# Performance work log

Hardware: AMD Instinct MI355X
Metric: run time of the kernel (lower is better)

The kernel has to match this reference:

```python
import jax, jax.numpy as jnp
import numpy as np

TOKENS = 32768
D_MODEL = 4096
N_EXPERTS = 64
BALANCE_LOSS_WEIGHT = 0.1


def setup_inputs() -> dict:
    key = jax.random.key(0)
    kx, kw1, kw2, kn = jax.random.split(key, 4)
    x = jax.random.normal(kx, (TOKENS, D_MODEL), dtype=jnp.float32)
    # torch nn.Linear weight layout: [out_features, in_features]
    w1 = jax.random.normal(kw1, (N_EXPERTS, D_MODEL), dtype=jnp.float32) / np.sqrt(D_MODEL)
    w2 = jax.random.normal(kw2, (N_EXPERTS, N_EXPERTS), dtype=jnp.float32) / np.sqrt(N_EXPERTS)
    # fixed Gumbel noise sample: g = -log(-log(u)), matching gumbel_rsample
    u = jax.random.uniform(kn, (TOKENS, N_EXPERTS), dtype=jnp.float32, minval=1e-8, maxval=1.0)
    noise = -jnp.log(-jnp.log(u))
    return {"x": x, "w1": w1, "w2": w2, "noise": noise}


def reference(x, w1, w2, noise):
    # MLP gate: Linear(d->E, no bias) -> tanh -> Linear(E->E, no bias)
    h = jnp.tanh(x @ w1.T)                       # [T, E]
    logits = h @ w2.T                             # [T, E]
    scores = jax.nn.softmax(logits, axis=1)       # [T, E]
    logits_w_noise = logits + noise               # gumbel-perturbed logits
    top1_indices = jnp.argmax(logits_w_noise, axis=1)   # [T] int
    top1_scores = jnp.max(logits_w_noise, axis=1)       # [T]
    # balance loss
    importance_mean = scores.mean(axis=0)                        # [E]
    load = jnp.bincount(top1_indices, length=N_EXPERTS)          # [E] int
    load_mean = load.astype(scores.dtype) / x.shape[0]           # [E]
    balance_loss = (N_EXPERTS * jnp.sum(importance_mean * load_mean)
                    * BALANCE_LOSS_WEIGHT)
    return (top1_indices, top1_scores, balance_loss, load_mean, importance_mean)
```

## Files before the change

kernel.cpp:

```cpp
#include <hip/hip_runtime.h>
#include <math.h>

#define TOKENS 32768
#define DM 4096
#define NE 64
#define BALW 0.1f

#define TG 64
#define GBLOCKS (TOKENS / TG)

typedef __attribute__((ext_vector_type(8))) short short8;
typedef __attribute__((ext_vector_type(4))) float f32x4;

typedef unsigned short us;

__device__ inline us bf16r(float f) {
  const unsigned u = __float_as_uint(f);
  return (us)((u + 0x7FFFu + ((u >> 16) & 1u)) >> 16);
}
__device__ inline float bf16f(us s) {
  return __uint_as_float(((unsigned)s) << 16);
}
__device__ inline void split8(const float4 v0, const float4 v1, short8& H,
                              short8& M, short8& L) {
  float v[8] = {v0.x, v0.y, v0.z, v0.w, v1.x, v1.y, v1.z, v1.w};
#pragma unroll
  for (int j = 0; j < 8; ++j) {
    const us hs = bf16r(v[j]);
    const float r1 = v[j] - bf16f(hs);
    const us ms = bf16r(r1);
    const float r2 = r1 - bf16f(ms);
    const us ls = bf16r(r2);
    H[j] = (short)hs; M[j] = (short)ms; L[j] = (short)ls;
  }
}

#define MFMA(a, b, c) __builtin_amdgcn_mfma_f32_16x16x32_bf16(a, b, c, 0, 0, 0)

__global__ void prep_w1_kernel(const float* __restrict__ w1,
                               us* __restrict__ bws) {
  const int kc = blockIdx.x;
  const int tid = threadIdx.x;
  const int ns = tid >> 6;
  const int l = tid & 63;
  const int r = l & 15, g = l >> 4;
  const int n = 16 * ns + r;
  const int kb = 32 * kc + 8 * g;
  const float* src = &w1[(size_t)n * DM + kb];
  const float4 v0 = *reinterpret_cast<const float4*>(src);
  const float4 v1 = *reinterpret_cast<const float4*>(src + 4);
  short8 H, M, L;
  split8(v0, v1, H, M, L);
  us* dst = bws + ((size_t)(kc * 4 + ns) * 3) * 512 + l * 8;
  *reinterpret_cast<short8*>(dst) = H;
  *reinterpret_cast<short8*>(dst + 512) = M;
  *reinterpret_cast<short8*>(dst + 1024) = L;
}

#define TMM 128

template <int SK>
__global__ __launch_bounds__(256, 3) void gemm_mfma_kernel(
    const float* __restrict__ x, const us* __restrict__ bws,
    float* __restrict__ hp) {
  constexpr int KS = DM / SK;
  constexpr int NIT = KS / 32;
  const int tid = threadIdx.x;
  const int kz = blockIdx.x % SK;
  const int mb = blockIdx.x / SK;
  const int w = tid >> 6;
  const int l = tid & 63;
  const int r = l & 15, g = l >> 4;
  const int row0 = mb * TMM + w * 32;
  const int kb0 = kz * KS;

  f32x4 acc[2][4];
#pragma unroll
  for (int i = 0; i < 2; ++i)
#pragma unroll
    for (int j = 0; j < 4; ++j) acc[i][j] = (f32x4)(0.f);

  const float* xA0 = &x[(size_t)(row0 + r) * DM + kb0 + 8 * g];
  const float* xA1 = xA0 + (size_t)16 * DM;
  const us* bb = bws + (size_t)(kb0 / 32) * 12 * 512 + l * 8;

  for (int it = 0; it < NIT; ++it) {
    const int koff = it * 32;
    const float4 a00 = *reinterpret_cast<const float4*>(xA0 + koff);
    const float4 a01 = *reinterpret_cast<const float4*>(xA0 + koff + 4);
    const float4 a10 = *reinterpret_cast<const float4*>(xA1 + koff);
    const float4 a11 = *reinterpret_cast<const float4*>(xA1 + koff + 4);
    const us* bt = bb + (size_t)it * 12 * 512;
    short8 bf[4][3];
#pragma unroll
    for (int ns = 0; ns < 4; ++ns)
#pragma unroll
      for (int p = 0; p < 3; ++p)
        bf[ns][p] =
            *reinterpret_cast<const short8*>(bt + (ns * 3 + p) * 512);

    short8 ah, am, al;
    split8(a00, a01, ah, am, al);
#pragma unroll
    for (int ns = 0; ns < 4; ++ns) {
      f32x4 c = acc[0][ns];
      c = MFMA(ah, bf[ns][0], c);
      c = MFMA(ah, bf[ns][1], c);
      c = MFMA(am, bf[ns][0], c);
      c = MFMA(ah, bf[ns][2], c);
      c = MFMA(am, bf[ns][1], c);
      c = MFMA(al, bf[ns][0], c);
      c = MFMA(am, bf[ns][2], c);
      c = MFMA(al, bf[ns][1], c);
      acc[0][ns] = c;
    }
    split8(a10, a11, ah, am, al);
#pragma unroll
    for (int ns = 0; ns < 4; ++ns) {
      f32x4 c = acc[1][ns];
      c = MFMA(ah, bf[ns][0], c);
      c = MFMA(ah, bf[ns][1], c);
      c = MFMA(am, bf[ns][0], c);
      c = MFMA(ah, bf[ns][2], c);
      c = MFMA(am, bf[ns][1], c);
      c = MFMA(al, bf[ns][0], c);
      c = MFMA(am, bf[ns][2], c);
      c = MFMA(al, bf[ns][1], c);
      acc[1][ns] = c;
    }
  }

  float* dst = hp + (size_t)kz * TOKENS * NE;
#pragma unroll
  for (int ms = 0; ms < 2; ++ms)
#pragma unroll
    for (int ns = 0; ns < 4; ++ns)
#pragma unroll
      for (int q = 0; q < 4; ++q)
        dst[(size_t)(row0 + 16 * ms + 4 * g + q) * NE + 16 * ns + r] =
            acc[ms][ns][q];
}

#define TM 128
#define BK 32
#define LDSA 132
#define LDSB 68

template <int SK>
__global__ __launch_bounds__(256, 4) void gemm_fp32_kernel(
    const float* __restrict__ x, const float* __restrict__ w1,
    float* __restrict__ hp) {
  constexpr int KS = DM / SK;
  __shared__ float As[BK * LDSA];
  __shared__ float Ws[BK * LDSB];
  const int tid = threadIdx.x;
  const int kz = blockIdx.x % SK;
  const int mb = blockIdx.x / SK;
  const int row0 = mb * TM;
  const int kbase = kz * KS;
  const int m0 = (tid >> 3) * 4;
  const int n0 = (tid & 7) * 8;
  const int rS = tid >> 2;
  const int kS = (tid & 3) * 4;

  float acc[4][8];
#pragma unroll
  for (int i = 0; i < 4; ++i)
#pragma unroll
    for (int j = 0; j < 8; ++j) acc[i][j] = 0.f;

  float4 ra[4], rw[2];
  const float* xp = &x[(size_t)(row0 + rS) * DM + kS];
  const float* wp = &w1[(size_t)rS * DM + kS];

#define LOAD_TILE(KC)                                                   \
  do {                                                                  \
    ra[0] = *reinterpret_cast<const float4*>(xp + (KC));                \
    ra[1] = *reinterpret_cast<const float4*>(xp + (KC) + 16);           \
    ra[2] = *reinterpret_cast<const float4*>(xp + (size_t)64 * DM + (KC));\
    ra[3] = *reinterpret_cast<const float4*>(xp + (size_t)64 * DM + (KC) + 16);\
    rw[0] = *reinterpret_cast<const float4*>(wp + (KC));                \
    rw[1] = *reinterpret_cast<const float4*>(wp + (KC) + 16);           \
  } while (0)

#define ST4(arr, stride, krow, col, v)                                  \
  do {                                                                  \
    arr[((krow) + 0) * (stride) + (col)] = (v).x;                       \
    arr[((krow) + 1) * (stride) + (col)] = (v).y;                       \
    arr[((krow) + 2) * (stride) + (col)] = (v).z;                       \
    arr[((krow) + 3) * (stride) + (col)] = (v).w;                       \
  } while (0)

#define STORE_TILE()                                                    \
  do {                                                                  \
    ST4(As, LDSA, kS, rS, ra[0]);                                       \
    ST4(As, LDSA, kS + 16, rS, ra[1]);                                  \
    ST4(As, LDSA, kS, rS + 64, ra[2]);                                  \
    ST4(As, LDSA, kS + 16, rS + 64, ra[3]);                             \
    ST4(Ws, LDSB, kS, rS, rw[0]);                                       \
    ST4(Ws, LDSB, kS + 16, rS, rw[1]);                                  \
  } while (0)

  LOAD_TILE(kbase);

  for (int kc = kbase; kc < kbase + KS; kc += BK) {
    __syncthreads();
    STORE_TILE();
    __syncthreads();
    if (kc + BK < kbase + KS) LOAD_TILE(kc + BK);
#pragma unroll 8
    for (int k = 0; k < BK; ++k) {
      const float4 a0 = *reinterpret_cast<const float4*>(&As[k * LDSA + m0]);
      const float4 b0 = *reinterpret_cast<const float4*>(&Ws[k * LDSB + n0]);
      const float4 b1 =
          *reinterpret_cast<const float4*>(&Ws[k * LDSB + n0 + 4]);
      const float a[4] = {a0.x, a0.y, a0.z, a0.w};
      const float b[8] = {b0.x, b0.y, b0.z, b0.w, b1.x, b1.y, b1.z, b1.w};
#pragma unroll
      for (int i = 0; i < 4; ++i)
#pragma unroll
        for (int j = 0; j < 8; ++j) acc[i][j] = fmaf(a[i], b[j], acc[i][j]);
    }
  }
#undef LOAD_TILE
#undef ST4
#undef STORE_TILE

  float* dst = hp + (size_t)kz * TOKENS * NE;
#pragma unroll
  for (int i = 0; i < 4; ++i) {
    const size_t o = (size_t)(row0 + m0 + i) * NE;
    *reinterpret_cast<float4*>(&dst[o + n0]) =
        make_float4(acc[i][0], acc[i][1], acc[i][2], acc[i][3]);
    *reinterpret_cast<float4*>(&dst[o + n0 + 4]) =
        make_float4(acc[i][4], acc[i][5], acc[i][6], acc[i][7]);
  }
}

template <int SK>
__global__ __launch_bounds__(256) void gate_kernel(
    const float* __restrict__ hp, const float* __restrict__ w2,
    const float* __restrict__ noise, float* __restrict__ out_idx,
    float* __restrict__ out_score, float* __restrict__ imp_part,
    float* __restrict__ load_part) {
  __shared__ float hs[TG * 65];
  __shared__ float w2s[NE * 65];
  __shared__ float ls[TG * 66];
  __shared__ float csum[2 * NE];
  __shared__ int hist[NE];
  const int tid = threadIdx.x;
  const int t0 = blockIdx.x * TG;
  if (tid < NE) hist[tid] = 0;

#pragma unroll
  for (int it = 0; it < 4; ++it) {
    const int f = tid + 256 * it;
    const int c = f & 15;
    const int t = f >> 4;
    const size_t g = (size_t)(t0 + t) * NE + c * 4;
    float4 p = *reinterpret_cast<const float4*>(&hp[g]);
#pragma unroll
    for (int s = 1; s < SK; ++s) {
      const float4 q =
          *reinterpret_cast<const float4*>(&hp[(size_t)s * TOKENS * NE + g]);
      p.x += q.x; p.y += q.y; p.z += q.z; p.w += q.w;
    }
    float* d = &hs[t * 65 + c * 4];
    d[0] = tanhf(p.x);
    d[1] = tanhf(p.y);
    d[2] = tanhf(p.z);
    d[3] = tanhf(p.w);
  }
#pragma unroll
  for (int it = 0; it < 4; ++it) {
    const int f = tid + 256 * it;
    const int c = f & 15;
    const int rr = f >> 4;
    const float4 v =
        *reinterpret_cast<const float4*>(&w2[(size_t)rr * NE + c * 4]);
    float* d = &w2s[rr * 65 + c * 4];
    d[0] = v.x; d[1] = v.y; d[2] = v.z; d[3] = v.w;
  }
  __syncthreads();

  {
    const int m0 = (tid >> 4) * 4;
    const int n0 = (tid & 15) * 4;
    float acc[4][4];
#pragma unroll
    for (int i = 0; i < 4; ++i)
#pragma unroll
      for (int j = 0; j < 4; ++j) acc[i][j] = 0.f;
#pragma unroll 8
    for (int k = 0; k < NE; ++k) {
      float a[4], b[4];
#pragma unroll
      for (int i = 0; i < 4; ++i) a[i] = hs[(m0 + i) * 65 + k];
#pragma unroll
      for (int j = 0; j < 4; ++j) b[j] = w2s[(n0 + j) * 65 + k];
#pragma unroll
      for (int i = 0; i < 4; ++i)
#pragma unroll
        for (int j = 0; j < 4; ++j) acc[i][j] = fmaf(a[i], b[j], acc[i][j]);
    }
#pragma unroll
    for (int i = 0; i < 4; ++i)
#pragma unroll
      for (int j = 0; j < 4; ++j) ls[(m0 + i) * 66 + n0 + j] = acc[i][j];
  }
  __syncthreads();

  if (tid < TG) {
    const int t = tid;
    float mx = -INFINITY, best = -INFINITY;
    int bi = 0;
    for (int e = 0; e < NE; ++e) {
      const float lv = ls[t * 66 + e];
      mx = fmaxf(mx, lv);
      const float gg = lv + noise[(size_t)(t0 + t) * NE + e];
      if (gg > best) { best = gg; bi = e; }
    }
    float s = 0.f;
    for (int e = 0; e < NE; ++e) {
      const float ex = expf(ls[t * 66 + e] - mx);
      s += ex;
      ls[t * 66 + e] = ex;
    }
    const float inv = 1.f / s;
    for (int e = 0; e < NE; ++e) ls[t * 66 + e] *= inv;
    out_idx[t0 + t] = (float)bi;
    out_score[t0 + t] = best;
    atomicAdd(&hist[bi], 1);
  }
  __syncthreads();

  if (tid < 128) {
    const int e = tid & 63;
    const int half = tid >> 6;
    float s = 0.f;
    for (int rr = half * 32; rr < half * 32 + 32; ++rr) s += ls[rr * 66 + e];
    csum[half * NE + e] = s;
  }
  __syncthreads();
  if (tid < NE) {
    imp_part[(size_t)blockIdx.x * NE + tid] = csum[tid] + csum[NE + tid];
    load_part[(size_t)blockIdx.x * NE + tid] = (float)hist[tid];
  }
}

__global__ void finalize_kernel(const float* __restrict__ imp_part,
                                const float* __restrict__ load_part,
                                float* __restrict__ out) {
  const int e = threadIdx.x;
  float imp = 0.f, ld = 0.f;
  for (int b = 0; b < GBLOCKS; ++b) {
    imp += imp_part[(size_t)b * NE + e];
    ld += load_part[(size_t)b * NE + e];
  }
  const float imp_mean = imp / (float)TOKENS;
  const float load_mean = ld / (float)TOKENS;
  out[2 * TOKENS + 1 + e] = load_mean;
  out[2 * TOKENS + 1 + NE + e] = imp_mean;
  float prod = imp_mean * load_mean;
#pragma unroll
  for (int off = 32; off > 0; off >>= 1) prod += __shfl_down(prod, off);
  if (e == 0) out[2 * TOKENS] = (float)NE * prod * BALW;
}

extern "C" void kernel_launch(void* const* d_in, const int* in_sizes, int n_in,
                              void* d_out, int out_size, void* d_ws,
                              size_t ws_size, hipStream_t stream) {
  const float* x = (const float*)d_in[0];
  const float* w1 = (const float*)d_in[1];
  const float* w2 = (const float*)d_in[2];
  const float* noise = (const float*)d_in[3];
  float* out = (float*)d_out;

  const size_t bws_shorts = (size_t)128 * 4 * 3 * 512;
  const size_t part_elems = (size_t)2 * GBLOCKS * NE;
  const size_t need_mfma = bws_shorts * sizeof(us) +
                           ((size_t)4 * TOKENS * NE + part_elems) *
                               sizeof(float);
  const size_t need_fp32 =
      ((size_t)2 * TOKENS * NE + part_elems) * sizeof(float);

  if (ws_size == 0 || ws_size >= need_mfma) {
    us* bws = (us*)d_ws;
    float* hp = (float*)(bws + bws_shorts);
    float* imp_part = hp + (size_t)4 * TOKENS * NE;
    float* load_part = imp_part + (size_t)GBLOCKS * NE;
    hipLaunchKernelGGL(prep_w1_kernel, dim3(128), dim3(256), 0, stream, w1,
                       bws);
    hipLaunchKernelGGL((gemm_mfma_kernel<4>), dim3((TOKENS / TMM) * 4),
                       dim3(256), 0, stream, x, bws, hp);
    hipLaunchKernelGGL((gate_kernel<4>), dim3(GBLOCKS), dim3(256), 0, stream,
                       hp, w2, noise, out, out + TOKENS, imp_part, load_part);
    hipLaunchKernelGGL(finalize_kernel, dim3(1), dim3(64), 0, stream, imp_part,
                       load_part, out);
  } else if (ws_size >= need_fp32) {
    float* hp = (float*)d_ws;
    float* imp_part = hp + (size_t)2 * TOKENS * NE;
    float* load_part = imp_part + (size_t)GBLOCKS * NE;
    hipLaunchKernelGGL((gemm_fp32_kernel<2>), dim3((TOKENS / TM) * 2),
                       dim3(256), 0, stream, x, w1, hp);
    hipLaunchKernelGGL((gate_kernel<2>), dim3(GBLOCKS), dim3(256), 0, stream,
                       hp, w2, noise, out, out + TOKENS, imp_part, load_part);
    hipLaunchKernelGGL(finalize_kernel, dim3(1), dim3(64), 0, stream, imp_part,
                       load_part, out);
  }
}
```

Before: 218.1 us.

## Prefetch next x tile, truncate-split bf16, and interleave MFMA chains in gate GEMM

The x tile for the next k-iteration is now loaded one iteration ahead (software pipelining) so global load latency overlaps the current MFMAs. The three-way bf16 split now uses truncation plus v_perm packing instead of round-to-nearest conversion, which cuts VALU work per element. The MFMA issue order is reordered to interleave the four independent accumulators, hiding MFMA dependency latency. Truncation changes the rounding of the hi/mid/lo terms, though the three-term split should still keep near-fp32 accuracy. Holding the extra prefetch registers adds register pressure.

```diff
diff --git a/kernel.cpp b/kernel.cpp
--- a/kernel.cpp
+++ b/kernel.cpp
@@ -33,6 +33,28 @@
     const us ls = bf16r(r2);
     H[j] = (short)hs; M[j] = (short)ms; L[j] = (short)ls;
   }
+}
+
+__device__ inline void split8t(const float4 v0, const float4 v1, short8& H,
+                               short8& M, short8& L) {
+  unsigned u[8], um[8], ul[8];
+  const float v[8] = {v0.x, v0.y, v0.z, v0.w, v1.x, v1.y, v1.z, v1.w};
+#pragma unroll
+  for (int j = 0; j < 8; ++j) {
+    u[j] = __float_as_uint(v[j]);
+    const float r1 = v[j] - __uint_as_float(u[j] & 0xFFFF0000u);
+    um[j] = __float_as_uint(r1);
+    const float r2 = r1 - __uint_as_float(um[j] & 0xFFFF0000u);
+    ul[j] = __float_as_uint(r2);
+  }
+  union Cvt { unsigned u4[4]; short8 s8; } h, m, l;
+#pragma unroll
+  for (int d = 0; d < 4; ++d) {
+    h.u4[d] = __builtin_amdgcn_perm(u[2 * d + 1], u[2 * d], 0x07060302u);
+    m.u4[d] = __builtin_amdgcn_perm(um[2 * d + 1], um[2 * d], 0x07060302u);
+    l.u4[d] = __builtin_amdgcn_perm(ul[2 * d + 1], ul[2 * d], 0x07060302u);
+  }
+  H = h.s8; M = m.s8; L = l.s8;
 }
 
 #define MFMA(a, b, c) __builtin_amdgcn_mfma_f32_16x16x32_bf16(a, b, c, 0, 0, 0)
@@ -84,12 +106,12 @@
   const float* xA1 = xA0 + (size_t)16 * DM;
   const us* bb = bws + (size_t)(kb0 / 32) * 12 * 512 + l * 8;
 
+  float4 a00 = *reinterpret_cast<const float4*>(xA0);
+  float4 a01 = *reinterpret_cast<const float4*>(xA0 + 4);
+  float4 a10 = *reinterpret_cast<const float4*>(xA1);
+  float4 a11 = *reinterpret_cast<const float4*>(xA1 + 4);
+
   for (int it = 0; it < NIT; ++it) {
-    const int koff = it * 32;
-    const float4 a00 = *reinterpret_cast<const float4*>(xA0 + koff);
-    const float4 a01 = *reinterpret_cast<const float4*>(xA0 + koff + 4);
-    const float4 a10 = *reinterpret_cast<const float4*>(xA1 + koff);
-    const float4 a11 = *reinterpret_cast<const float4*>(xA1 + koff + 4);
     const us* bt = bb + (size_t)it * 12 * 512;
     short8 bf[4][3];
 #pragma unroll
@@ -99,35 +121,40 @@
         bf[ns][p] =
             *reinterpret_cast<const short8*>(bt + (ns * 3 + p) * 512);
 
+    const int ko = ((it + 1 < NIT) ? it + 1 : it) * 32;
+    const float4 n00 = *reinterpret_cast<const float4*>(xA0 + ko);
+    const float4 n01 = *reinterpret_cast<const float4*>(xA0 + ko + 4);
+    const float4 n10 = *reinterpret_cast<const float4*>(xA1 + ko);
+    const float4 n11 = *reinterpret_cast<const float4*>(xA1 + ko + 4);
+
     short8 ah, am, al;
-    split8(a00, a01, ah, am, al);
-#pragma unroll
-    for (int ns = 0; ns < 4; ++ns) {
-      f32x4 c = acc[0][ns];
-      c = MFMA(ah, bf[ns][0], c);
-      c = MFMA(ah, bf[ns][1], c);
-      c = MFMA(am, bf[ns][0], c);
-      c = MFMA(ah, bf[ns][2], c);
-      c = MFMA(am, bf[ns][1], c);
-      c = MFMA(al, bf[ns][0], c);
-      c = MFMA(am, bf[ns][2], c);
-      c = MFMA(al, bf[ns][1], c);
-      acc[0][ns] = c;
-    }
-    split8(a10, a11, ah, am, al);
-#pragma unroll
-    for (int ns = 0; ns < 4; ++ns) {
-      f32x4 c = acc[1][ns];
-      c = MFMA(ah, bf[ns][0], c);
-      c = MFMA(ah, bf[ns][1], c);
-      c = MFMA(am, bf[ns][0], c);
-      c = MFMA(ah, bf[ns][2], c);
-      c = MFMA(am, bf[ns][1], c);
-      c = MFMA(al, bf[ns][0], c);
-      c = MFMA(am, bf[ns][2], c);
-      c = MFMA(al, bf[ns][1], c);
-      acc[1][ns] = c;
-    }
+#define TERMS(H_)                                                        \
+  do {                                                                   \
+    _Pragma("unroll") for (int ns = 0; ns < 4; ++ns) acc[H_][ns] =       \
+        MFMA(ah, bf[ns][0], acc[H_][ns]);                                \
+    _Pragma("unroll") for (int ns = 0; ns < 4; ++ns) acc[H_][ns] =       \
+        MFMA(ah, bf[ns][1], acc[H_][ns]);                                \
+    _Pragma("unroll") for (int ns = 0; ns < 4; ++ns) acc[H_][ns] =       \
+        MFMA(am, bf[ns][0], acc[H_][ns]);                                \
+    _Pragma("unroll") for (int ns = 0; ns < 4; ++ns) acc[H_][ns] =       \
+        MFMA(ah, bf[ns][2], acc[H_][ns]);                                \
+    _Pragma("unroll") for (int ns = 0; ns < 4; ++ns) acc[H_][ns] =       \
+        MFMA(am, bf[ns][1], acc[H_][ns]);                                \
+    _Pragma("unroll") for (int ns = 0; ns < 4; ++ns) acc[H_][ns] =       \
+        MFMA(al, bf[ns][0], acc[H_][ns]);                                \
+    _Pragma("unroll") for (int ns = 0; ns < 4; ++ns) acc[H_][ns] =       \
+        MFMA(am, bf[ns][2], acc[H_][ns]);                                \
+    _Pragma("unroll") for (int ns = 0; ns < 4; ++ns) acc[H_][ns] =       \
+        MFMA(al, bf[ns][1], acc[H_][ns]);                                \
+  } while (0)
+
+    split8t(a00, a01, ah, am, al);
+    TERMS(0);
+    split8t(a10, a11, ah, am, al);
+    TERMS(1);
+#undef TERMS
+
+    a00 = n00; a01 = n01; a10 = n10; a11 = n11;
   }
 
   float* dst = hp + (size_t)kz * TOKENS * NE;
```

New measurement: 205.8 us. 1.06x faster.
